# Optimization experiments

Hardware: AMD Instinct MI355X
Metric: run time of the kernel (lower is better)

Reference implementation:

```python
import jax, jax.numpy as jnp
import numpy as np

CAPACITY_FACTOR = 1.0  # fairseq Top1Gate default


def setup_inputs() -> dict:
    key = jax.random.key(0)
    ks = jax.random.split(key, 5)
    B, T, M, H, O, E = 8, 1024, 1024, 4096, 1024, 4
    return {
        "hidden_states": jax.random.normal(ks[0], (B, T, M), jnp.float32),
        "gate_w": jax.random.normal(ks[1], (M, E), jnp.float32) * 0.02,
        "fc1_w": jax.random.normal(ks[2], (E, M, H), jnp.float32) * 0.02,
        "fc1_b": jnp.zeros((E, H), jnp.float32),
        "fc2_w": jax.random.normal(ks[3], (E, H, O), jnp.float32) * 0.02,
        "fc2_b": jnp.zeros((E, O), jnp.float32),
    }


def reference(hidden_states, gate_w, fc1_w, fc1_b, fc2_w, fc2_b):
    B, T, M = hidden_states.shape
    E = gate_w.shape[1]
    S = B * T
    C = int(CAPACITY_FACTOR * -(-S // E))  # ceil(S/E)

    features = hidden_states.reshape(S, M)  # [S, M]

    # ---- Top1 gate (fairseq top1gating, eval path: no shuffle/noise) ----
    logits = features @ gate_w                      # [S, E]
    gates = jax.nn.softmax(logits, axis=1)          # [S, E]
    idx = jnp.argmax(gates, axis=1)                 # [S]
    mask1 = jax.nn.one_hot(idx, E, dtype=gates.dtype)  # [S, E]

    # load-balancing aux loss (computed before capacity dropping)
    me = jnp.mean(gates, axis=0)
    ce = jnp.mean(mask1, axis=0)
    l_aux = jnp.sum(me * ce) * E

    # capacity: position within each expert's queue; drop overflow tokens
    locations = jnp.cumsum(mask1, axis=0) - 1.0     # [S, E]
    mask1 = mask1 * (locations < C)
    loc_s = jnp.sum(locations * mask1, axis=1).astype(jnp.int32)  # [S]
    gates1_s = jnp.sum(gates * mask1, axis=1)       # [S] gate value (0 if dropped)

    # combine_weights [S, E, C] and boolean dispatch mask (as float for mm)
    combine = (gates1_s[:, None, None] * mask1[:, :, None]
               * jax.nn.one_hot(loc_s, C, dtype=gates.dtype)[:, None, :])
    dispatch = (combine > 0).astype(features.dtype)  # [S, E, C]

    # ---- dispatch via dense one-hot matmul: [E*C, S] @ [S, M] ----
    dispatch_ecs = jnp.transpose(dispatch, (1, 2, 0)).reshape(E * C, S)
    dispatched = (dispatch_ecs @ features).reshape(E, C, M)

    # ---- per-expert MLP (grouped GEMM) ----
    h = jax.nn.gelu(jnp.einsum('ecm,emh->ech', dispatched, fc1_w) + fc1_b[:, None, :])
    expert_out = jnp.einsum('ech,eho->eco', h, fc2_w) + fc2_b[:, None, :]  # [E, C, O]

    # ---- combine via dense matmul: [S, E*C] @ [E*C, O] ----
    O = expert_out.shape[-1]
    combined = combine.reshape(S, E * C) @ expert_out.reshape(E * C, O)

    return combined.reshape(B, T, O), l_aux
```

## Files before the change

### kernel.cpp

```cpp
#include <hip/hip_runtime.h>
#include <stdint.h>

#define S_TOK 8192
#define MDIM  1024
#define HDIM  4096
#define ODIM  1024
#define NEXP  4
#define CAP   2048

typedef __attribute__((ext_vector_type(8))) short short8;
typedef __attribute__((ext_vector_type(4))) float floatx4;

__device__ __forceinline__ unsigned short f2bf(float x) {
  union { float f; unsigned u; } v; v.f = x;
  unsigned r = v.u + 0x7FFFu + ((v.u >> 16) & 1u);
  return (unsigned short)(r >> 16);
}

__device__ __forceinline__ void gl_lds16(const void* g, void* l) {
  __builtin_amdgcn_global_load_lds(
      (const __attribute__((address_space(1))) void*)g,
      (__attribute__((address_space(3))) void*)l, 16, 0, 0);
}

__device__ __forceinline__ float gelu_tanh(float x) {
  float p = x * x;
  float t = x * (1.5957691216f + 0.0713548353f * p);
  float E = __expf(-t);
  return __fdividef(x, 1.0f + E);
}

__device__ __forceinline__ const char* stage_src(const char* base, int linoff,
                                                 int rowstride) {
  int row  = linoff >> 6;
  int slot = (linoff >> 4) & 3;
  int c16  = slot ^ ((row >> 1) & 3);
  return base + (size_t)row * rowstride + (c16 << 4);
}

__global__ __launch_bounds__(256) void prep_kernel(
    const float* __restrict__ feat, const float* __restrict__ gw,
    const float* __restrict__ w1,
    int* __restrict__ idx, float* __restrict__ gval, float* __restrict__ gsum,
    unsigned short* __restrict__ wt, float* __restrict__ outz)
{
  __shared__ float bs[4];
  __shared__ unsigned short tile[64][66];
  const int bid = blockIdx.x;

  if (bid < 2048) {
    int wave = threadIdx.x >> 6, lane = threadIdx.x & 63;
    int s = bid * 4 + wave;
    const float4* f4 = (const float4*)(feat + (size_t)s * MDIM);
    double a0 = 0, a1 = 0, a2 = 0, a3 = 0;
    #pragma unroll
    for (int j = 0; j < 4; ++j) {
      int m4 = lane + j * 64;
      float4 x = f4[m4];
      #pragma unroll
      for (int c = 0; c < 4; ++c) {
        float xv = (c == 0) ? x.x : (c == 1) ? x.y : (c == 2) ? x.z : x.w;
        float4 w = ((const float4*)gw)[m4 * 4 + c];
        a0 += (double)xv * w.x; a1 += (double)xv * w.y;
        a2 += (double)xv * w.z; a3 += (double)xv * w.w;
      }
    }
    #pragma unroll
    for (int off = 32; off; off >>= 1) {
      a0 += __shfl_down(a0, off); a1 += __shfl_down(a1, off);
      a2 += __shfl_down(a2, off); a3 += __shfl_down(a3, off);
    }
    if (threadIdx.x < 4) bs[threadIdx.x] = 0.f;
    __syncthreads();
    if (lane == 0) {
      double lg[4] = {a0, a1, a2, a3};
      double mx = lg[0]; int bi = 0;
      #pragma unroll
      for (int e = 1; e < 4; ++e) if (lg[e] > mx) { mx = lg[e]; bi = e; }
      float ex[4]; float den = 0.f;
      #pragma unroll
      for (int e = 0; e < 4; ++e) { ex[e] = __expf((float)(lg[e] - mx)); den += ex[e]; }
      float inv = 1.f / den;
      idx[s]  = bi;
      gval[s] = ex[bi] * inv;
      #pragma unroll
      for (int e = 0; e < 4; ++e) atomicAdd(&bs[e], ex[e] * inv);
    }
    __syncthreads();
    if (threadIdx.x < 4) atomicAdd(&gsum[threadIdx.x], bs[threadIdx.x]);
  } else if (bid < 2048 + 4096) {
    int t = bid - 2048;
    int bz = t >> 10, rem = t & 1023;
    int bx = rem & 63, by = rem >> 6;
    const float* in = w1 + (size_t)bz * MDIM * HDIM;
    unsigned short* out = wt + (size_t)bz * MDIM * HDIM;
    int c0 = bx * 64, r0 = by * 64;
    int tx = threadIdx.x & 15, ty = threadIdx.x >> 4;
    #pragma unroll
    for (int p = 0; p < 4; ++p) {
      int r = ty + p * 16;
      float4 v = *(const float4*)(in + (size_t)(r0 + r) * HDIM + c0 + tx * 4);
      tile[r][tx * 4 + 0] = f2bf(v.x);
      tile[r][tx * 4 + 1] = f2bf(v.y);
      tile[r][tx * 4 + 2] = f2bf(v.z);
      tile[r][tx * 4 + 3] = f2bf(v.w);
    }
    __syncthreads();
    #pragma unroll
    for (int p = 0; p < 4; ++p) {
      int c = ty + p * 16;
      ushort4 o;
      o.x = tile[tx * 4 + 0][c];
      o.y = tile[tx * 4 + 1][c];
      o.z = tile[tx * 4 + 2][c];
      o.w = tile[tx * 4 + 3][c];
      *(ushort4*)(out + (size_t)(c0 + c) * MDIM + r0 + tx * 4) = o;
    }
  } else {
    int t = bid - (2048 + 4096);
    float4* p = (float4*)(outz + (size_t)t * 4096) + threadIdx.x;
    float4 z = {0.f, 0.f, 0.f, 0.f};
    #pragma unroll
    for (int q = 0; q < 4; ++q) p[q * 256] = z;
  }
}

__global__ __launch_bounds__(1024) void scan_kernel(
    const int* __restrict__ idx, int* __restrict__ perm,
    int* __restrict__ ne, const float* __restrict__ gsum,
    float* __restrict__ laux)
{
  const int tid = threadIdx.x, wave = tid >> 6, lane = tid & 63;
  __shared__ int cnt[16][4];
  __shared__ int off[16][4];
  __shared__ int tot[4];
  unsigned long long below = (lane == 0) ? 0ull : ((~0ull) >> (64 - lane));

  int myE[8], loc[8];
  int c[4] = {0, 0, 0, 0};
  #pragma unroll
  for (int j = 0; j < 8; ++j) {
    int s = wave * 512 + j * 64 + lane;
    int ev = idx[s];
    myE[j] = ev;
    #pragma unroll
    for (int e = 0; e < 4; ++e) {
      unsigned long long mb = __ballot(ev == e);
      if (ev == e) loc[j] = c[e] + __popcll(mb & below);
      c[e] += __popcll(mb);
    }
  }
  if (lane == 0) {
    #pragma unroll
    for (int e = 0; e < 4; ++e) cnt[wave][e] = c[e];
  }
  __syncthreads();
  if (tid < 64) {
    int w = tid >> 2, e = tid & 3;
    int o = 0;
    for (int w2 = 0; w2 < 16; ++w2) if (w2 < w) o += cnt[w2][e];
    off[w][e] = o;
    if (w == 15) tot[e] = o + cnt[15][e];
  }
  __syncthreads();
  #pragma unroll
  for (int j = 0; j < 8; ++j) {
    int s = wave * 512 + j * 64 + lane;
    int e = myE[j];
    int rank = off[wave][e] + loc[j];
    if (rank < CAP) perm[e * CAP + rank] = s;
  }
  if (tid < 4) ne[tid] = tot[tid] < CAP ? tot[tid] : CAP;
  if (tid == 0) {
    float l = 0.f;
    #pragma unroll
    for (int e = 0; e < 4; ++e)
      l += (gsum[e] * (1.0f / S_TOK)) * ((float)tot[e] * (1.0f / S_TOK));
    *laux = l * (float)NEXP;
  }
}

__global__ __launch_bounds__(256) void transpose_cast(
    const float* __restrict__ in, unsigned short* __restrict__ out, int R, int Cc)
{
  __shared__ unsigned short tile[64][66];
  in  += (size_t)blockIdx.z * R * Cc;
  out += (size_t)blockIdx.z * R * Cc;
  int c0 = blockIdx.x * 64, r0 = blockIdx.y * 64;
  int tx = threadIdx.x & 15;
  int ty = threadIdx.x >> 4;
  #pragma unroll
  for (int p = 0; p < 4; ++p) {
    int r = ty + p * 16;
    float4 v = *(const float4*)(in + (size_t)(r0 + r) * Cc + c0 + tx * 4);
    tile[r][tx * 4 + 0] = f2bf(v.x);
    tile[r][tx * 4 + 1] = f2bf(v.y);
    tile[r][tx * 4 + 2] = f2bf(v.z);
    tile[r][tx * 4 + 3] = f2bf(v.w);
  }
  __syncthreads();
  #pragma unroll
  for (int p = 0; p < 4; ++p) {
    int c = ty + p * 16;
    ushort4 o;
    o.x = tile[tx * 4 + 0][c];
    o.y = tile[tx * 4 + 1][c];
    o.z = tile[tx * 4 + 2][c];
    o.w = tile[tx * 4 + 3][c];
    *(ushort4*)(out + (size_t)(c0 + c) * R + r0 + tx * 4) = o;
  }
}

__global__ __launch_bounds__(256) void gather_kernel(
    const float* __restrict__ feat, const int* __restrict__ perm,
    const int* __restrict__ ne, unsigned short* __restrict__ disp)
{
  int b = blockIdx.x;
  int e = b >> 11, c = b & (CAP - 1);
  int m = threadIdx.x * 4;
  ushort4 o;
  if (c < ne[e]) {
    int s = perm[b];
    float4 v = *(const float4*)(feat + (size_t)s * MDIM + m);
    o.x = f2bf(v.x); o.y = f2bf(v.y); o.z = f2bf(v.z); o.w = f2bf(v.w);
  } else {
    o.x = o.y = o.z = o.w = 0;
  }
  *(ushort4*)(disp + (size_t)b * MDIM + m) = o;
}

__global__ __launch_bounds__(256) void fc1_kernel(
    const unsigned short* __restrict__ A, const unsigned short* __restrict__ Bt,
    const float* __restrict__ b1, unsigned short* __restrict__ Hb)
{
  const int nb = blockIdx.x, mb = blockIdx.y, e = blockIdx.z;
  const int tid = threadIdx.x, wave = tid >> 6, lane = tid & 63;

  __shared__ __align__(16) unsigned short smA[3 * 128 * 32];
  __shared__ __align__(16) unsigned short smB[3 * 128 * 32];

  const char* Ag = (const char*)(A + ((size_t)e * CAP + (size_t)mb * 128) * MDIM);
  const char* Bg = (const char*)(Bt + ((size_t)e * HDIM + (size_t)nb * 128) * MDIM);

  const int boff0 = (wave * 2 + 0) * 1024 + lane * 16;
  const int boff1 = (wave * 2 + 1) * 1024 + lane * 16;
  const char* agp0 = stage_src(Ag, boff0, 2048);
  const char* agp1 = stage_src(Ag, boff1, 2048);
  const char* bgp0 = stage_src(Bg, boff0, 2048);
  const char* bgp1 = stage_src(Bg, boff1, 2048);
  const int ldsw0 = (wave * 2 + 0) * 512;
  const int ldsw1 = (wave * 2 + 1) * 512;

  const int wm = (wave & 1) * 64, wn = (wave >> 1) * 64;
  const int fr = lane & 15, fq = lane >> 4;
  const int sqA = ((fq ^ ((wm + fr) >> 1)) & 3) * 8;
  const int sqB = ((fq ^ ((wn + fr) >> 1)) & 3) * 8;

  floatx4 acc[4][4] = {};

  auto stage = [&](int kb, int bo) {
    gl_lds16(agp0 + kb, smA + bo + ldsw0);
    gl_lds16(agp1 + kb, smA + bo + ldsw1);
    gl_lds16(bgp0 + kb, smB + bo + ldsw0);
    gl_lds16(bgp1 + kb, smB + bo + ldsw1);
  };
  auto comp = [&](const unsigned short* sA, const unsigned short* sB) {
    short8 af[4], bfr[4];
    #pragma unroll
    for (int i = 0; i < 4; ++i)
      af[i] = *(const short8*)&sA[(wm + i * 16 + fr) * 32 + sqA];
    #pragma unroll
    for (int j = 0; j < 4; ++j)
      bfr[j] = *(const short8*)&sB[(wn + j * 16 + fr) * 32 + sqB];
    #pragma unroll
    for (int i = 0; i < 4; ++i)
      #pragma unroll
      for (int j = 0; j < 4; ++j)
        acc[i][j] = __builtin_amdgcn_mfma_f32_16x16x32_bf16(bfr[j], af[i], acc[i][j], 0, 0, 0);
  };

  const int NT = MDIM / 32;
  stage(0, 0); stage(64, 4096);
  asm volatile("s_waitcnt vmcnt(4)" ::: "memory");
  __builtin_amdgcn_s_barrier();

  for (int kt = 0; kt < NT - 2; kt += 3) {
    stage((kt + 2) * 64, 2 * 4096); comp(smA, smB);
    asm volatile("s_waitcnt vmcnt(4)" ::: "memory"); __builtin_amdgcn_s_barrier();
    stage((kt + 3) * 64, 0 * 4096); comp(smA + 4096, smB + 4096);
    asm volatile("s_waitcnt vmcnt(4)" ::: "memory"); __builtin_amdgcn_s_barrier();
    stage((kt + 4) * 64, 1 * 4096); comp(smA + 8192, smB + 8192);
    asm volatile("s_waitcnt vmcnt(4)" ::: "memory"); __builtin_amdgcn_s_barrier();
  }
  comp(smA, smB);
  asm volatile("s_waitcnt vmcnt(0)" ::: "memory");
  __builtin_amdgcn_s_barrier();
  comp(smA + 4096, smB + 4096);

  unsigned short* Hrow = Hb + (size_t)e * CAP * HDIM;
  #pragma unroll
  for (int j = 0; j < 4; ++j) {
    int gn0 = nb * 128 + wn + j * 16 + fq * 4;
    float4 bv = *(const float4*)&b1[e * HDIM + gn0];
    #pragma unroll
    for (int i = 0; i < 4; ++i) {
      int m = mb * 128 + wm + i * 16 + fr;
      ushort4 o;
      o.x = f2bf(gelu_tanh(acc[i][j][0] + bv.x));
      o.y = f2bf(gelu_tanh(acc[i][j][1] + bv.y));
      o.z = f2bf(gelu_tanh(acc[i][j][2] + bv.z));
      o.w = f2bf(gelu_tanh(acc[i][j][3] + bv.w));
      *(ushort4*)&Hrow[(size_t)m * HDIM + gn0] = o;
    }
  }
}

__global__ __launch_bounds__(256) void fc2_kernel(
    const unsigned short* __restrict__ A, const unsigned short* __restrict__ Bt,
    const float* __restrict__ b2, const int* __restrict__ perm,
    const int* __restrict__ ne, const float* __restrict__ gval,
    float* __restrict__ out)
{
  const int b = blockIdx.x;
  const int wg = (b & 7) * 128 + (b >> 3);
  const int nb = wg & 7, mb = (wg >> 3) & 31, e = wg >> 8;
  const int tid = threadIdx.x, wave = tid >> 6, lane = tid & 63;

  __shared__ __align__(16) unsigned short smA[3 * 64 * 32];
  __shared__ __align__(16) unsigned short smB[3 * 128 * 32];

  const char* Ag = (const char*)(A + ((size_t)e * CAP + (size_t)mb * 64) * HDIM);
  const char* Bg = (const char*)(Bt + ((size_t)e * ODIM + (size_t)nb * 128) * HDIM);

  const char* agp = stage_src(Ag, tid * 16, 8192);
  const int boff0 = (wave * 2 + 0) * 1024 + lane * 16;
  const int boff1 = (wave * 2 + 1) * 1024 + lane * 16;
  const char* bgp0 = stage_src(Bg, boff0, 8192);
  const char* bgp1 = stage_src(Bg, boff1, 8192);

  const int ldsA_w = wave * 512;
  const int ldsB_w0 = (wave * 2 + 0) * 512;
  const int ldsB_w1 = (wave * 2 + 1) * 512;

  const int wm = (wave & 1) * 32, wn = (wave >> 1) * 64;
  const int fr = lane & 15, fq = lane >> 4;
  const int sqA = ((fq ^ ((wm + fr) >> 1)) & 3) * 8;
  const int sqB = ((fq ^ ((wn + fr) >> 1)) & 3) * 8;

  floatx4 acc[2][4] = {};

  auto stage = [&](int kb, int boA, int boB) {
    gl_lds16(agp + kb,  smA + boA + ldsA_w);
    gl_lds16(bgp0 + kb, smB + boB + ldsB_w0);
    gl_lds16(bgp1 + kb, smB + boB + ldsB_w1);
  };
  auto comp = [&](const unsigned short* sA, const unsigned short* sB) {
    short8 af[2], bfr[4];
    #pragma unroll
    for (int i = 0; i < 2; ++i)
      af[i] = *(const short8*)&sA[(wm + i * 16 + fr) * 32 + sqA];
    #pragma unroll
    for (int j = 0; j < 4; ++j)
      bfr[j] = *(const short8*)&sB[(wn + j * 16 + fr) * 32 + sqB];
    #pragma unroll
    for (int i = 0; i < 2; ++i)
      #pragma unroll
      for (int j = 0; j < 4; ++j)
        acc[i][j] = __builtin_amdgcn_mfma_f32_16x16x32_bf16(bfr[j], af[i], acc[i][j], 0, 0, 0);
  };

  const int NT = HDIM / 32;
  stage(0, 0, 0); stage(64, 2048, 4096);
  asm volatile("s_waitcnt vmcnt(3)" ::: "memory");
  __builtin_amdgcn_s_barrier();

  for (int kt = 0; kt < NT - 2; kt += 3) {
    stage((kt + 2) * 64, 2 * 2048, 2 * 4096); comp(smA, smB);
    asm volatile("s_waitcnt vmcnt(3)" ::: "memory"); __builtin_amdgcn_s_barrier();
    stage((kt + 3) * 64, 0 * 2048, 0 * 4096); comp(smA + 2048, smB + 4096);
    asm volatile("s_waitcnt vmcnt(3)" ::: "memory"); __builtin_amdgcn_s_barrier();
    stage((kt + 4) * 64, 1 * 2048, 1 * 4096); comp(smA + 4096, smB + 8192);
    asm volatile("s_waitcnt vmcnt(3)" ::: "memory"); __builtin_amdgcn_s_barrier();
  }
  comp(smA, smB);
  asm volatile("s_waitcnt vmcnt(0)" ::: "memory");
  __builtin_amdgcn_s_barrier();
  comp(smA + 2048, smB + 4096);

  const int nE = ne[e];
  float4 b2v[4];
  #pragma unroll
  for (int j = 0; j < 4; ++j)
    b2v[j] = *(const float4*)&b2[e * ODIM + nb * 128 + wn + j * 16 + fq * 4];
  #pragma unroll
  for (int i = 0; i < 2; ++i) {
    int c = mb * 64 + wm + i * 16 + fr;
    if (c < nE) {
      int s = perm[e * CAP + c];
      float g = gval[s];
      float* orow = out + (size_t)s * ODIM + nb * 128 + wn + fq * 4;
      #pragma unroll
      for (int j = 0; j < 4; ++j) {
        float4 o;
        o.x = (acc[i][j][0] + b2v[j].x) * g;
        o.y = (acc[i][j][1] + b2v[j].y) * g;
        o.z = (acc[i][j][2] + b2v[j].z) * g;
        o.w = (acc[i][j][3] + b2v[j].w) * g;
        *(float4*)&orow[j * 16] = o;
      }
    }
  }
}

extern "C" void kernel_launch(void* const* d_in, const int* in_sizes, int n_in,
                              void* d_out, int out_size, void* d_ws, size_t ws_size,
                              hipStream_t stream) {
  const float* feat = (const float*)d_in[0];
  const float* gw   = (const float*)d_in[1];
  const float* w1   = (const float*)d_in[2];
  const float* b1   = (const float*)d_in[3];
  const float* w2   = (const float*)d_in[4];
  const float* b2   = (const float*)d_in[5];
  float* out = (float*)d_out;

  char* ws = (char*)d_ws;
  unsigned short* wt   = (unsigned short*)(ws);
  unsigned short* hbuf = (unsigned short*)(ws + 33554432);
  unsigned short* disp = (unsigned short*)(ws + 100663296);
  int*   idx  = (int*)  (ws + 117440512);
  float* gval = (float*)(ws + 117473280);
  int*   perm = (int*)  (ws + 117506048);
  float* gsum = (float*)(ws + 117538816);
  int*   ne   = (int*)  (ws + 117538832);

  hipMemsetAsync(ws + 117538816, 0, 32, stream);

  prep_kernel<<<2048 + 4096 + 2048, 256, 0, stream>>>(
      feat, gw, w1, idx, gval, gsum, wt, out);
  scan_kernel<<<1, 1024, 0, stream>>>(idx, perm, ne, gsum, out + (size_t)S_TOK * ODIM);
  gather_kernel<<<NEXP * CAP, 256, 0, stream>>>(feat, perm, ne, disp);
  fc1_kernel<<<dim3(HDIM / 128, CAP / 128, NEXP), 256, 0, stream>>>(disp, wt, b1, hbuf);
  transpose_cast<<<dim3(ODIM / 64, HDIM / 64, NEXP), 256, 0, stream>>>(w2, wt, HDIM, ODIM);
  fc2_kernel<<<1024, 256, 0, stream>>>(hbuf, wt, b2, perm, ne, gval, out);
}
```

Measured before the change: 416.3 us.

## Regroup prep kernels: fuse gather with weight casts and zeroing into one launch

New measurement: 440.7 us. 1.06x slower.

```diff
diff --git a/kernel.cpp b/kernel.cpp
--- a/kernel.cpp
+++ b/kernel.cpp
@@ -38,157 +38,12 @@
   return base + (size_t)row * rowstride + (c16 << 4);
 }
 
-__global__ __launch_bounds__(256) void prep_kernel(
-    const float* __restrict__ feat, const float* __restrict__ gw,
-    const float* __restrict__ w1,
-    int* __restrict__ idx, float* __restrict__ gval, float* __restrict__ gsum,
-    unsigned short* __restrict__ wt, float* __restrict__ outz)
-{
-  __shared__ float bs[4];
-  __shared__ unsigned short tile[64][66];
-  const int bid = blockIdx.x;
-
-  if (bid < 2048) {
-    int wave = threadIdx.x >> 6, lane = threadIdx.x & 63;
-    int s = bid * 4 + wave;
-    const float4* f4 = (const float4*)(feat + (size_t)s * MDIM);
-    double a0 = 0, a1 = 0, a2 = 0, a3 = 0;
-    #pragma unroll
-    for (int j = 0; j < 4; ++j) {
-      int m4 = lane + j * 64;
-      float4 x = f4[m4];
-      #pragma unroll
-      for (int c = 0; c < 4; ++c) {
-        float xv = (c == 0) ? x.x : (c == 1) ? x.y : (c == 2) ? x.z : x.w;
-        float4 w = ((const float4*)gw)[m4 * 4 + c];
-        a0 += (double)xv * w.x; a1 += (double)xv * w.y;
-        a2 += (double)xv * w.z; a3 += (double)xv * w.w;
-      }
-    }
-    #pragma unroll
-    for (int off = 32; off; off >>= 1) {
-      a0 += __shfl_down(a0, off); a1 += __shfl_down(a1, off);
-      a2 += __shfl_down(a2, off); a3 += __shfl_down(a3, off);
-    }
-    if (threadIdx.x < 4) bs[threadIdx.x] = 0.f;
-    __syncthreads();
-    if (lane == 0) {
-      double lg[4] = {a0, a1, a2, a3};
-      double mx = lg[0]; int bi = 0;
-      #pragma unroll
-      for (int e = 1; e < 4; ++e) if (lg[e] > mx) { mx = lg[e]; bi = e; }
-      float ex[4]; float den = 0.f;
-      #pragma unroll
-      for (int e = 0; e < 4; ++e) { ex[e] = __expf((float)(lg[e] - mx)); den += ex[e]; }
-      float inv = 1.f / den;
-      idx[s]  = bi;
-      gval[s] = ex[bi] * inv;
-      #pragma unroll
-      for (int e = 0; e < 4; ++e) atomicAdd(&bs[e], ex[e] * inv);
-    }
-    __syncthreads();
-    if (threadIdx.x < 4) atomicAdd(&gsum[threadIdx.x], bs[threadIdx.x]);
-  } else if (bid < 2048 + 4096) {
-    int t = bid - 2048;
-    int bz = t >> 10, rem = t & 1023;
-    int bx = rem & 63, by = rem >> 6;
-    const float* in = w1 + (size_t)bz * MDIM * HDIM;
-    unsigned short* out = wt + (size_t)bz * MDIM * HDIM;
-    int c0 = bx * 64, r0 = by * 64;
-    int tx = threadIdx.x & 15, ty = threadIdx.x >> 4;
-    #pragma unroll
-    for (int p = 0; p < 4; ++p) {
-      int r = ty + p * 16;
-      float4 v = *(const float4*)(in + (size_t)(r0 + r) * HDIM + c0 + tx * 4);
-      tile[r][tx * 4 + 0] = f2bf(v.x);
-      tile[r][tx * 4 + 1] = f2bf(v.y);
-      tile[r][tx * 4 + 2] = f2bf(v.z);
-      tile[r][tx * 4 + 3] = f2bf(v.w);
-    }
-    __syncthreads();
-    #pragma unroll
-    for (int p = 0; p < 4; ++p) {
-      int c = ty + p * 16;
-      ushort4 o;
-      o.x = tile[tx * 4 + 0][c];
-      o.y = tile[tx * 4 + 1][c];
-      o.z = tile[tx * 4 + 2][c];
-      o.w = tile[tx * 4 + 3][c];
-      *(ushort4*)(out + (size_t)(c0 + c) * MDIM + r0 + tx * 4) = o;
-    }
-  } else {
-    int t = bid - (2048 + 4096);
-    float4* p = (float4*)(outz + (size_t)t * 4096) + threadIdx.x;
-    float4 z = {0.f, 0.f, 0.f, 0.f};
-    #pragma unroll
-    for (int q = 0; q < 4; ++q) p[q * 256] = z;
-  }
-}
-
-__global__ __launch_bounds__(1024) void scan_kernel(
-    const int* __restrict__ idx, int* __restrict__ perm,
-    int* __restrict__ ne, const float* __restrict__ gsum,
-    float* __restrict__ laux)
-{
-  const int tid = threadIdx.x, wave = tid >> 6, lane = tid & 63;
-  __shared__ int cnt[16][4];
-  __shared__ int off[16][4];
-  __shared__ int tot[4];
-  unsigned long long below = (lane == 0) ? 0ull : ((~0ull) >> (64 - lane));
-
-  int myE[8], loc[8];
-  int c[4] = {0, 0, 0, 0};
-  #pragma unroll
-  for (int j = 0; j < 8; ++j) {
-    int s = wave * 512 + j * 64 + lane;
-    int ev = idx[s];
-    myE[j] = ev;
-    #pragma unroll
-    for (int e = 0; e < 4; ++e) {
-      unsigned long long mb = __ballot(ev == e);
-      if (ev == e) loc[j] = c[e] + __popcll(mb & below);
-      c[e] += __popcll(mb);
-    }
-  }
-  if (lane == 0) {
-    #pragma unroll
-    for (int e = 0; e < 4; ++e) cnt[wave][e] = c[e];
-  }
-  __syncthreads();
-  if (tid < 64) {
-    int w = tid >> 2, e = tid & 3;
-    int o = 0;
-    for (int w2 = 0; w2 < 16; ++w2) if (w2 < w) o += cnt[w2][e];
-    off[w][e] = o;
-    if (w == 15) tot[e] = o + cnt[15][e];
-  }
-  __syncthreads();
-  #pragma unroll
-  for (int j = 0; j < 8; ++j) {
-    int s = wave * 512 + j * 64 + lane;
-    int e = myE[j];
-    int rank = off[wave][e] + loc[j];
-    if (rank < CAP) perm[e * CAP + rank] = s;
-  }
-  if (tid < 4) ne[tid] = tot[tid] < CAP ? tot[tid] : CAP;
-  if (tid == 0) {
-    float l = 0.f;
-    #pragma unroll
-    for (int e = 0; e < 4; ++e)
-      l += (gsum[e] * (1.0f / S_TOK)) * ((float)tot[e] * (1.0f / S_TOK));
-    *laux = l * (float)NEXP;
-  }
-}
-
-__global__ __launch_bounds__(256) void transpose_cast(
-    const float* __restrict__ in, unsigned short* __restrict__ out, int R, int Cc)
-{
-  __shared__ unsigned short tile[64][66];
-  in  += (size_t)blockIdx.z * R * Cc;
-  out += (size_t)blockIdx.z * R * Cc;
-  int c0 = blockIdx.x * 64, r0 = blockIdx.y * 64;
-  int tx = threadIdx.x & 15;
-  int ty = threadIdx.x >> 4;
+__device__ __forceinline__ void tcast64(
+    const float* __restrict__ in, unsigned short* __restrict__ out,
+    int R, int Cc, int bx, int by, unsigned short (*tile)[66])
+{
+  int c0 = bx * 64, r0 = by * 64;
+  int tx = threadIdx.x & 15, ty = threadIdx.x >> 4;
   #pragma unroll
   for (int p = 0; p < 4; ++p) {
     int r = ty + p * 16;
@@ -211,22 +66,165 @@
   }
 }
 
-__global__ __launch_bounds__(256) void gather_kernel(
+__global__ __launch_bounds__(256) void gate_kernel(
+    const float* __restrict__ feat, const float* __restrict__ gw,
+    int* __restrict__ idx, float* __restrict__ gval, float* __restrict__ gsum)
+{
+  int wave = threadIdx.x >> 6, lane = threadIdx.x & 63;
+  int s = blockIdx.x * 4 + wave;
+  const float4* f4 = (const float4*)(feat + (size_t)s * MDIM);
+  double a0 = 0, a1 = 0, a2 = 0, a3 = 0;
+  #pragma unroll
+  for (int j = 0; j < 4; ++j) {
+    int m4 = lane + j * 64;
+    float4 x = f4[m4];
+    #pragma unroll
+    for (int c = 0; c < 4; ++c) {
+      float xv = (c == 0) ? x.x : (c == 1) ? x.y : (c == 2) ? x.z : x.w;
+      float4 w = ((const float4*)gw)[m4 * 4 + c];
+      a0 += (double)xv * w.x; a1 += (double)xv * w.y;
+      a2 += (double)xv * w.z; a3 += (double)xv * w.w;
+    }
+  }
+  #pragma unroll
+  for (int off = 32; off; off >>= 1) {
+    a0 += __shfl_down(a0, off); a1 += __shfl_down(a1, off);
+    a2 += __shfl_down(a2, off); a3 += __shfl_down(a3, off);
+  }
+  __shared__ float bs[4];
+  if (threadIdx.x < 4) bs[threadIdx.x] = 0.f;
+  __syncthreads();
+  if (lane == 0) {
+    double lg[4] = {a0, a1, a2, a3};
+    double mx = lg[0]; int bi = 0;
+    #pragma unroll
+    for (int e = 1; e < 4; ++e) if (lg[e] > mx) { mx = lg[e]; bi = e; }
+    float ex[4]; float den = 0.f;
+    #pragma unroll
+    for (int e = 0; e < 4; ++e) { ex[e] = __expf((float)(lg[e] - mx)); den += ex[e]; }
+    float inv = 1.f / den;
+    idx[s]  = bi;
+    gval[s] = ex[bi] * inv;
+    #pragma unroll
+    for (int e = 0; e < 4; ++e) atomicAdd(&bs[e], ex[e] * inv);
+  }
+  __syncthreads();
+  if (threadIdx.x < 4) atomicAdd(&gsum[threadIdx.x], bs[threadIdx.x]);
+}
+
+__global__ __launch_bounds__(1024) void scan_kernel(
+    const int* __restrict__ idx, int* __restrict__ perm,
+    int* __restrict__ ne, const float* __restrict__ gsum,
+    float* __restrict__ laux)
+{
+  const int tid = threadIdx.x, wave = tid >> 6, lane = tid & 63;
+  __shared__ int cnt[16][4];
+  __shared__ int off[16][4];
+  __shared__ int tot[4];
+  unsigned long long below = (lane == 0) ? 0ull : ((~0ull) >> (64 - lane));
+
+  int myE[8], loc[8];
+  int c[4] = {0, 0, 0, 0};
+  #pragma unroll
+  for (int j = 0; j < 8; ++j) {
+    int s = wave * 512 + j * 64 + lane;
+    int ev = idx[s];
+    myE[j] = ev;
+    #pragma unroll
+    for (int e = 0; e < 4; ++e) {
+      unsigned long long mb = __ballot(ev == e);
+      if (ev == e) loc[j] = c[e] + __popcll(mb & below);
+      c[e] += __popcll(mb);
+    }
+  }
+  if (lane == 0) {
+    #pragma unroll
+    for (int e = 0; e < 4; ++e) cnt[wave][e] = c[e];
+  }
+  __syncthreads();
+  if (tid < 64) {
+    int w = tid >> 2, e = tid & 3;
+    int o = 0;
+    for (int w2 = 0; w2 < 16; ++w2) if (w2 < w) o += cnt[w2][e];
+    off[w][e] = o;
+    if (w == 15) tot[e] = o + cnt[15][e];
+  }
+  __syncthreads();
+  #pragma unroll
+  for (int j = 0; j < 8; ++j) {
+    int s = wave * 512 + j * 64 + lane;
+    int e = myE[j];
+    int rank = off[wave][e] + loc[j];
+    if (rank < CAP) perm[e * CAP + rank] = s;
+  }
+  if (tid < 4) ne[tid] = tot[tid] < CAP ? tot[tid] : CAP;
+  if (tid == 0) {
+    float l = 0.f;
+    #pragma unroll
+    for (int e = 0; e < 4; ++e)
+      l += (gsum[e] * (1.0f / S_TOK)) * ((float)tot[e] * (1.0f / S_TOK));
+    *laux = l * (float)NEXP;
+  }
+}
+
+__global__ __launch_bounds__(256) void mid_kernel(
     const float* __restrict__ feat, const int* __restrict__ perm,
-    const int* __restrict__ ne, unsigned short* __restrict__ disp)
-{
-  int b = blockIdx.x;
-  int e = b >> 11, c = b & (CAP - 1);
-  int m = threadIdx.x * 4;
-  ushort4 o;
-  if (c < ne[e]) {
-    int s = perm[b];
-    float4 v = *(const float4*)(feat + (size_t)s * MDIM + m);
-    o.x = f2bf(v.x); o.y = f2bf(v.y); o.z = f2bf(v.z); o.w = f2bf(v.w);
-  } else {
-    o.x = o.y = o.z = o.w = 0;
-  }
-  *(ushort4*)(disp + (size_t)b * MDIM + m) = o;
+    const int* __restrict__ ne, unsigned short* __restrict__ disp,
+    const float* __restrict__ w1, unsigned short* __restrict__ wt,
+    const float* __restrict__ w2, unsigned short* __restrict__ w2t,
+    int has_w2t, float* __restrict__ outz)
+{
+  __shared__ unsigned short tile[64][66];
+  int bid = blockIdx.x;
+
+  if (bid < NEXP * CAP) {
+    int e = bid >> 11, c = bid & (CAP - 1);
+    int m = threadIdx.x * 4;
+    ushort4 o;
+    if (c < ne[e]) {
+      int s = perm[bid];
+      float4 v = *(const float4*)(feat + (size_t)s * MDIM + m);
+      o.x = f2bf(v.x); o.y = f2bf(v.y); o.z = f2bf(v.z); o.w = f2bf(v.w);
+    } else {
+      o.x = o.y = o.z = o.w = 0;
+    }
+    *(ushort4*)(disp + (size_t)bid * MDIM + m) = o;
+    return;
+  }
+  bid -= NEXP * CAP;
+
+  if (bid < 4096) {
+    int bz = bid >> 10, rem = bid & 1023;
+    int bx = rem & 63, by = rem >> 6;
+    tcast64(w1 + (size_t)bz * MDIM * HDIM, wt + (size_t)bz * MDIM * HDIM,
+            MDIM, HDIM, bx, by, tile);
+    return;
+  }
+  bid -= 4096;
+
+  if (has_w2t) {
+    if (bid < 4096) {
+      int bz = bid >> 10, rem = bid & 1023;
+      int bx = rem & 15, by = rem >> 4;
+      tcast64(w2 + (size_t)bz * HDIM * ODIM, w2t + (size_t)bz * HDIM * ODIM,
+              HDIM, ODIM, bx, by, tile);
+      return;
+    }
+    bid -= 4096;
+  }
+
+  float4* p = (float4*)(outz + (size_t)bid * 4096) + threadIdx.x;
+  float4 z = {0.f, 0.f, 0.f, 0.f};
+  #pragma unroll
+  for (int q = 0; q < 4; ++q) p[q * 256] = z;
+}
+
+__global__ __launch_bounds__(256) void transpose_cast(
+    const float* __restrict__ in, unsigned short* __restrict__ out, int R, int Cc)
+{
+  __shared__ unsigned short tile[64][66];
+  tcast64(in + (size_t)blockIdx.z * R * Cc, out + (size_t)blockIdx.z * R * Cc,
+          R, Cc, blockIdx.x, blockIdx.y, tile);
 }
 
 __global__ __launch_bounds__(256) void fc1_kernel(
@@ -433,13 +431,20 @@
   float* gsum = (float*)(ws + 117538816);
   int*   ne   = (int*)  (ws + 117538832);
 
+  const size_t W2T_OFF = 117571584;
+  const size_t W2T_NEED = W2T_OFF + (size_t)NEXP * HDIM * ODIM * 2;
+  int has_w2t = (ws_size >= W2T_NEED);
+  unsigned short* w2t = has_w2t ? (unsigned short*)(ws + W2T_OFF) : wt;
+
   hipMemsetAsync(ws + 117538816, 0, 32, stream);
 
-  prep_kernel<<<2048 + 4096 + 2048, 256, 0, stream>>>(
-      feat, gw, w1, idx, gval, gsum, wt, out);
+  gate_kernel<<<S_TOK / 4, 256, 0, stream>>>(feat, gw, idx, gval, gsum);
   scan_kernel<<<1, 1024, 0, stream>>>(idx, perm, ne, gsum, out + (size_t)S_TOK * ODIM);
-  gather_kernel<<<NEXP * CAP, 256, 0, stream>>>(feat, perm, ne, disp);
+  int mid_grid = NEXP * CAP + 4096 + (has_w2t ? 4096 : 0) + 2048;
+  mid_kernel<<<mid_grid, 256, 0, stream>>>(
+      feat, perm, ne, disp, w1, wt, w2, w2t, has_w2t, out);
   fc1_kernel<<<dim3(HDIM / 128, CAP / 128, NEXP), 256, 0, stream>>>(disp, wt, b1, hbuf);
-  transpose_cast<<<dim3(ODIM / 64, HDIM / 64, NEXP), 256, 0, stream>>>(w2, wt, HDIM, ODIM);
-  fc2_kernel<<<1024, 256, 0, stream>>>(hbuf, wt, b2, perm, ne, gval, out);
-}
+  if (!has_w2t)
+    transpose_cast<<<dim3(ODIM / 64, HDIM / 64, NEXP), 256, 0, stream>>>(w2, wt, HDIM, ODIM);
+  fc2_kernel<<<1024, 256, 0, stream>>>(hbuf, w2t, b2, perm, ne, gval, out);
+}
```
